# Kernel optimization log

Measured on AMD Instinct MI355X. Metric: run time of the kernel, lower is better.

Reference implementation:

```python
import jax, jax.numpy as jnp
import numpy as np

N = 4194304  # number of sequential steps (batch dim scanned over)


def setup_inputs() -> dict:
    key = jax.random.key(0)
    k1, k2, k3 = jax.random.split(key, 3)
    x = jax.random.normal(k1, (N, 1, 3), dtype=jnp.float32)
    update = jax.random.normal(k2, (N, 3, 1), dtype=jnp.float32)
    # torch init: (-1-1)*rand([3,1]) + 1  -> uniform in (-1, 1]
    network0 = -2.0 * jax.random.uniform(k3, (3, 1), dtype=jnp.float32) + 1.0
    return {"x": x, "update": update, "network0": network0}


def reference(x, update, network0):
    # state s: [3,1] fast-weight vector
    # per step: s <- sigmoid(10*(s + update_i - 0.5)); pred_i = x_i[0,:] @ s
    def step(s, inp):
        xi, ui = inp  # xi: [1,3], ui: [3,1]
        s = jax.nn.sigmoid(10.0 * (s + ui - 0.5))
        pred = (xi @ s)[0]  # [1,3]@[3,1] -> [1,1] -> [1]
        return s, pred

    _, preds = jax.lax.scan(step, network0, (x, update))
    return preds  # [N, 1]
```

## Files before the change

### kernel.cpp

```cpp
#include <hip/hip_runtime.h>

#define CH 32
#define TPB 256

__device__ __forceinline__ float sig10(float s, float u) {
    float t = (s + u) - 0.5f;
    float a = 10.0f * t;
    float e = __expf(-a);
    return 1.0f / (1.0f + e);
}

__device__ __forceinline__ void step3(float& s0, float& s1, float& s2,
                                      float u0, float u1, float u2) {
    s0 = sig10(s0, u0); s1 = sig10(s1, u1); s2 = sig10(s2, u2);
}

__global__ void __launch_bounds__(TPB, 2) p1_bracket(
    const float* __restrict__ update, float* __restrict__ state_in,
    int* __restrict__ flags, int* __restrict__ blockflags, int C, int N) {
  __shared__ int s_w[TPB / 64];
  const int tid = threadIdx.x;
  if (tid < TPB / 64) s_w[tid] = 0;
  __syncthreads();
  const int c = blockIdx.x * TPB + tid;
  const bool have = (c < C);
  const bool full = have && ((size_t)(c + 1) * CH <= (size_t)N);
  int flag = 0;
  float a0 = 0.f, a1 = 0.f, a2 = 0.f;
  if (full) {
    const float4* up4 = (const float4*)(update + (size_t)c * (CH * 3));
    float4 u[24];
#pragma unroll
    for (int g = 0; g < 24; ++g) u[g] = up4[g];
    const float lo = (c == 0) ? -1.0f : 0.0f;
    a0 = a1 = a2 = lo;
    float b0 = 1.f, b1 = 1.f, b2 = 1.f;
    bool bdone = false;
#pragma unroll
    for (int g = 0; g < 8; ++g) {
      const float4 A = u[3 * g], B = u[3 * g + 1], Cv = u[3 * g + 2];
      step3(a0, a1, a2, A.x, A.y, A.z);
      step3(a0, a1, a2, A.w, B.x, B.y);
      step3(a0, a1, a2, B.z, B.w, Cv.x);
      step3(a0, a1, a2, Cv.y, Cv.z, Cv.w);
      if (!bdone) {
        step3(b0, b1, b2, A.x, A.y, A.z);
        step3(b0, b1, b2, A.w, B.x, B.y);
        step3(b0, b1, b2, B.z, B.w, Cv.x);
        step3(b0, b1, b2, Cv.y, Cv.z, Cv.w);
        bdone = __all((a0 == b0) && (a1 == b1) && (a2 == b2));
      }
    }
    flag = bdone ? 0 : 1;
  } else if (have) {
    const float* up = update + (size_t)c * (CH * 3);
    int steps = N - c * CH;
    const float lo = (c == 0) ? -1.0f : 0.0f;
    a0 = a1 = a2 = lo;
    float b0 = 1.f, b1 = 1.f, b2 = 1.f;
    for (int i = 0; i < steps; ++i) {
      step3(a0, a1, a2, up[3 * i], up[3 * i + 1], up[3 * i + 2]);
      step3(b0, b1, b2, up[3 * i], up[3 * i + 1], up[3 * i + 2]);
    }
    flag = !((a0 == b0) && (a1 == b1) && (a2 == b2));
  }
  if (have) {
    if (c + 1 < C) {
      state_in[(size_t)(c + 1) * 3 + 0] = a0;
      state_in[(size_t)(c + 1) * 3 + 1] = a1;
      state_in[(size_t)(c + 1) * 3 + 2] = a2;
    }
    flags[c] = flag;
  }
  unsigned long long bal = __ballot(flag != 0);
  if ((tid & 63) == 0) s_w[tid >> 6] = (bal != 0ull) ? 1 : 0;
  __syncthreads();
  if (tid == 0) {
    int bf = 0;
#pragma unroll
    for (int w = 0; w < TPB / 64; ++w) bf |= s_w[w];
    blockflags[blockIdx.x] = bf;
  }
}

__global__ void p2_fix(const float* __restrict__ update,
                       const float* __restrict__ net0,
                       float* __restrict__ state_in,
                       const int* __restrict__ flags,
                       const int* __restrict__ blockflags,
                       int C, int N, int NBLK) {
  __shared__ int s_any;
  if (threadIdx.x == 0) s_any = 0;
  __syncthreads();
  int bad = 0;
  for (int i = threadIdx.x; i < NBLK; i += blockDim.x) bad |= blockflags[i];
  if (bad) atomicOr(&s_any, 1);
  __syncthreads();
  if (threadIdx.x != 0) return;
  const int any = s_any;

  float s0 = net0[0], s1 = net0[1], s2 = net0[2];
  state_in[0] = s0; state_in[1] = s1; state_in[2] = s2;
  {
    const float* up = update;
    int steps = min(CH, N);
    for (int i = 0; i < steps; ++i)
      step3(s0, s1, s2, up[3 * i], up[3 * i + 1], up[3 * i + 2]);
    if (C > 1) { state_in[3] = s0; state_in[4] = s1; state_in[5] = s2; }
  }
  if (!any) return;
  for (int blk = 0; blk < NBLK; ++blk) {
    if (!blockflags[blk]) continue;
    int cc0 = blk * TPB; if (cc0 == 0) cc0 = 1;
    int cc1 = min(blk * TPB + TPB, C);
    for (int cc = cc0; cc < cc1; ++cc) {
      if (!flags[cc]) continue;
      float t0 = state_in[(size_t)cc * 3 + 0];
      float t1 = state_in[(size_t)cc * 3 + 1];
      float t2 = state_in[(size_t)cc * 3 + 2];
      const float* up = update + (size_t)cc * (CH * 3);
      int steps = min(CH, N - cc * CH);
      for (int i = 0; i < steps; ++i)
        step3(t0, t1, t2, up[3 * i], up[3 * i + 1], up[3 * i + 2]);
      if (cc + 1 < C) {
        state_in[(size_t)(cc + 1) * 3 + 0] = t0;
        state_in[(size_t)(cc + 1) * 3 + 1] = t1;
        state_in[(size_t)(cc + 1) * 3 + 2] = t2;
      }
    }
  }
}

__global__ void __launch_bounds__(TPB, 2) p3_emit(
    const float* __restrict__ x, const float* __restrict__ update,
    const float* __restrict__ state_in, float* __restrict__ out, int C, int N) {
  __shared__ float s_out[TPB * 33];
  const int tid = threadIdx.x;
  const int c = blockIdx.x * TPB + tid;
  const bool fullBlock = ((size_t)(blockIdx.x + 1) * (TPB * CH) <= (size_t)N);
  if (fullBlock) {
    const float4* up4 = (const float4*)(update + (size_t)c * (CH * 3));
    const float4* xp4 = (const float4*)(x + (size_t)c * (CH * 3));
    float s0 = state_in[(size_t)c * 3 + 0];
    float s1 = state_in[(size_t)c * 3 + 1];
    float s2 = state_in[(size_t)c * 3 + 2];
    float4 u[24], xv[24];
#pragma unroll
    for (int g = 0; g < 24; ++g) u[g] = up4[g];
#pragma unroll
    for (int g = 0; g < 24; ++g) xv[g] = xp4[g];
#pragma unroll
    for (int g = 0; g < 8; ++g) {
      const float4 UA = u[3 * g], UB = u[3 * g + 1], UC = u[3 * g + 2];
      const float4 XA = xv[3 * g], XB = xv[3 * g + 1], XC = xv[3 * g + 2];
      float o0, o1, o2, o3;
      step3(s0, s1, s2, UA.x, UA.y, UA.z); o0 = XA.x * s0 + XA.y * s1 + XA.z * s2;
      step3(s0, s1, s2, UA.w, UB.x, UB.y); o1 = XA.w * s0 + XB.x * s1 + XB.y * s2;
      step3(s0, s1, s2, UB.z, UB.w, UC.x); o2 = XB.z * s0 + XB.w * s1 + XC.x * s2;
      step3(s0, s1, s2, UC.y, UC.z, UC.w); o3 = XC.y * s0 + XC.z * s1 + XC.w * s2;
      s_out[tid * 33 + g * 4 + 0] = o0;
      s_out[tid * 33 + g * 4 + 1] = o1;
      s_out[tid * 33 + g * 4 + 2] = o2;
      s_out[tid * 33 + g * 4 + 3] = o3;
    }
    __syncthreads();
    float* ob = out + (size_t)blockIdx.x * (TPB * CH);
#pragma unroll
    for (int k = 0; k < 32; ++k) {
      int f = k * TPB + tid;
      int t = f >> 5, idx = f & 31;
      ob[f] = s_out[t * 33 + idx];
    }
  } else if (c < C) {
    float s0 = state_in[(size_t)c * 3 + 0];
    float s1 = state_in[(size_t)c * 3 + 1];
    float s2 = state_in[(size_t)c * 3 + 2];
    const float* up = update + (size_t)c * (CH * 3);
    const float* xp = x + (size_t)c * (CH * 3);
    float* op = out + (size_t)c * CH;
    int steps = min(CH, N - c * CH);
    for (int i = 0; i < steps; ++i) {
      step3(s0, s1, s2, up[3 * i], up[3 * i + 1], up[3 * i + 2]);
      op[i] = xp[3 * i] * s0 + xp[3 * i + 1] * s1 + xp[3 * i + 2] * s2;
    }
  }
}

extern "C" void kernel_launch(void* const* d_in, const int* in_sizes, int n_in,
                              void* d_out, int out_size, void* d_ws, size_t ws_size,
                              hipStream_t stream) {
    const float* x      = (const float*)d_in[0];
    const float* update = (const float*)d_in[1];
    const float* net0   = (const float*)d_in[2];
    float* out = (float*)d_out;
    int N = out_size;
    int C = (N + CH - 1) / CH;
    int nblk = (C + TPB - 1) / TPB;

    float* state_in = (float*)d_ws;
    int* flags = (int*)((char*)d_ws + (size_t)C * 3 * sizeof(float));
    int* blockflags = flags + C;

    hipLaunchKernelGGL(p1_bracket, dim3(nblk), dim3(TPB), 0, stream,
                       update, state_in, flags, blockflags, C, N);
    hipLaunchKernelGGL(p2_fix, dim3(1), dim3(1024), 0, stream,
                       update, net0, state_in, flags, blockflags, C, N, nblk);
    hipLaunchKernelGGL(p3_emit, dim3(nblk), dim3(TPB), 0, stream,
                       x, update, state_in, out, C, N);
}
```

Baseline: 151.3 us.

## Stage update and x tiles through swizzled LDS with coalesced loads, one wave per block

Replaces the per-thread strided float4 loads (each thread reading its own 384-byte chunk) with coalesced cooperative loads of the block's whole tile into shared memory, using an XOR swizzle to avoid bank conflicts. Threads then read their chunk from LDS. Blocks shrink to a single 64-lane wave, so the block flag comes straight from the ballot and the cross-wave shared reduction goes away. This adds LDS traffic and barriers, and the p2 fix pass now scans four times as many block flags.

```diff
diff --git a/kernel.cpp b/kernel.cpp
--- a/kernel.cpp
+++ b/kernel.cpp
@@ -1,7 +1,9 @@
 #include <hip/hip_runtime.h>
 
 #define CH 32
-#define TPB 256
+#define CPB 64
+#define F4C 24
+#define TILE (CPB * F4C)
 
 __device__ __forceinline__ float sig10(float s, float u) {
     float t = (s + u) - 0.5f;
@@ -15,30 +17,38 @@
     s0 = sig10(s0, u0); s1 = sig10(s1, u1); s2 = sig10(s2, u2);
 }
 
-__global__ void __launch_bounds__(TPB, 2) p1_bracket(
+__device__ __forceinline__ int swz(int F) { return F ^ ((F / F4C) & 7); }
+
+__global__ void p1_bracket(
     const float* __restrict__ update, float* __restrict__ state_in,
     int* __restrict__ flags, int* __restrict__ blockflags, int C, int N) {
-  __shared__ int s_w[TPB / 64];
-  const int tid = threadIdx.x;
-  if (tid < TPB / 64) s_w[tid] = 0;
-  __syncthreads();
-  const int c = blockIdx.x * TPB + tid;
-  const bool have = (c < C);
-  const bool full = have && ((size_t)(c + 1) * CH <= (size_t)N);
+  __shared__ float4 su[TILE];
+  const int lane = threadIdx.x;
+  const int blk  = blockIdx.x;
+  const int c    = blk * CPB + lane;
+  const bool blockFull = ((size_t)(blk + 1) * (CPB * CH) <= (size_t)N);
   int flag = 0;
   float a0 = 0.f, a1 = 0.f, a2 = 0.f;
-  if (full) {
-    const float4* up4 = (const float4*)(update + (size_t)c * (CH * 3));
-    float4 u[24];
-#pragma unroll
-    for (int g = 0; g < 24; ++g) u[g] = up4[g];
+
+  if (blockFull) {
+    const float4* up4 = (const float4*)update + (size_t)blk * TILE;
+    float4 raw[F4C];
+#pragma unroll
+    for (int ld = 0; ld < F4C; ++ld) raw[ld] = up4[ld * CPB + lane];
+#pragma unroll
+    for (int ld = 0; ld < F4C; ++ld) su[swz(ld * CPB + lane)] = raw[ld];
+    __syncthreads();
+
     const float lo = (c == 0) ? -1.0f : 0.0f;
     a0 = a1 = a2 = lo;
     float b0 = 1.f, b1 = 1.f, b2 = 1.f;
     bool bdone = false;
+    const int base = lane * F4C;
 #pragma unroll
     for (int g = 0; g < 8; ++g) {
-      const float4 A = u[3 * g], B = u[3 * g + 1], Cv = u[3 * g + 2];
+      const float4 A  = su[swz(base + 3 * g + 0)];
+      const float4 B  = su[swz(base + 3 * g + 1)];
+      const float4 Cv = su[swz(base + 3 * g + 2)];
       step3(a0, a1, a2, A.x, A.y, A.z);
       step3(a0, a1, a2, A.w, B.x, B.y);
       step3(a0, a1, a2, B.z, B.w, Cv.x);
@@ -52,9 +62,9 @@
       }
     }
     flag = bdone ? 0 : 1;
-  } else if (have) {
+  } else if (c < C) {
     const float* up = update + (size_t)c * (CH * 3);
-    int steps = N - c * CH;
+    int steps = min(CH, N - c * CH);
     const float lo = (c == 0) ? -1.0f : 0.0f;
     a0 = a1 = a2 = lo;
     float b0 = 1.f, b1 = 1.f, b2 = 1.f;
@@ -64,7 +74,8 @@
     }
     flag = !((a0 == b0) && (a1 == b1) && (a2 == b2));
   }
-  if (have) {
+
+  if (c < C) {
     if (c + 1 < C) {
       state_in[(size_t)(c + 1) * 3 + 0] = a0;
       state_in[(size_t)(c + 1) * 3 + 1] = a1;
@@ -73,14 +84,7 @@
     flags[c] = flag;
   }
   unsigned long long bal = __ballot(flag != 0);
-  if ((tid & 63) == 0) s_w[tid >> 6] = (bal != 0ull) ? 1 : 0;
-  __syncthreads();
-  if (tid == 0) {
-    int bf = 0;
-#pragma unroll
-    for (int w = 0; w < TPB / 64; ++w) bf |= s_w[w];
-    blockflags[blockIdx.x] = bf;
-  }
+  if (lane == 0) blockflags[blk] = (bal != 0ull) ? 1 : 0;
 }
 
 __global__ void p2_fix(const float* __restrict__ update,
@@ -111,8 +115,8 @@
   if (!any) return;
   for (int blk = 0; blk < NBLK; ++blk) {
     if (!blockflags[blk]) continue;
-    int cc0 = blk * TPB; if (cc0 == 0) cc0 = 1;
-    int cc1 = min(blk * TPB + TPB, C);
+    int cc0 = blk * CPB; if (cc0 == 0) cc0 = 1;
+    int cc1 = min(blk * CPB + CPB, C);
     for (int cc = cc0; cc < cc1; ++cc) {
       if (!flags[cc]) continue;
       float t0 = state_in[(size_t)cc * 3 + 0];
@@ -131,45 +135,63 @@
   }
 }
 
-__global__ void __launch_bounds__(TPB, 2) p3_emit(
+__global__ void p3_emit(
     const float* __restrict__ x, const float* __restrict__ update,
     const float* __restrict__ state_in, float* __restrict__ out, int C, int N) {
-  __shared__ float s_out[TPB * 33];
-  const int tid = threadIdx.x;
-  const int c = blockIdx.x * TPB + tid;
-  const bool fullBlock = ((size_t)(blockIdx.x + 1) * (TPB * CH) <= (size_t)N);
-  if (fullBlock) {
-    const float4* up4 = (const float4*)(update + (size_t)c * (CH * 3));
-    const float4* xp4 = (const float4*)(x + (size_t)c * (CH * 3));
+  __shared__ float4 su[TILE];
+  __shared__ float4 sx[TILE];
+  const int lane = threadIdx.x;
+  const int blk  = blockIdx.x;
+  const int c    = blk * CPB + lane;
+  const bool blockFull = ((size_t)(blk + 1) * (CPB * CH) <= (size_t)N);
+
+  if (blockFull) {
+    const float4* up4 = (const float4*)update + (size_t)blk * TILE;
+    const float4* xp4 = (const float4*)x      + (size_t)blk * TILE;
+    float4 ru[F4C], rx[F4C];
+#pragma unroll
+    for (int ld = 0; ld < F4C; ++ld) ru[ld] = up4[ld * CPB + lane];
+#pragma unroll
+    for (int ld = 0; ld < F4C; ++ld) rx[ld] = xp4[ld * CPB + lane];
+#pragma unroll
+    for (int ld = 0; ld < F4C; ++ld) su[swz(ld * CPB + lane)] = ru[ld];
+#pragma unroll
+    for (int ld = 0; ld < F4C; ++ld) sx[swz(ld * CPB + lane)] = rx[ld];
+    __syncthreads();
+
     float s0 = state_in[(size_t)c * 3 + 0];
     float s1 = state_in[(size_t)c * 3 + 1];
     float s2 = state_in[(size_t)c * 3 + 2];
-    float4 u[24], xv[24];
-#pragma unroll
-    for (int g = 0; g < 24; ++g) u[g] = up4[g];
-#pragma unroll
-    for (int g = 0; g < 24; ++g) xv[g] = xp4[g];
+    float obuf[CH];
+    const int base = lane * F4C;
 #pragma unroll
     for (int g = 0; g < 8; ++g) {
-      const float4 UA = u[3 * g], UB = u[3 * g + 1], UC = u[3 * g + 2];
-      const float4 XA = xv[3 * g], XB = xv[3 * g + 1], XC = xv[3 * g + 2];
-      float o0, o1, o2, o3;
-      step3(s0, s1, s2, UA.x, UA.y, UA.z); o0 = XA.x * s0 + XA.y * s1 + XA.z * s2;
-      step3(s0, s1, s2, UA.w, UB.x, UB.y); o1 = XA.w * s0 + XB.x * s1 + XB.y * s2;
-      step3(s0, s1, s2, UB.z, UB.w, UC.x); o2 = XB.z * s0 + XB.w * s1 + XC.x * s2;
-      step3(s0, s1, s2, UC.y, UC.z, UC.w); o3 = XC.y * s0 + XC.z * s1 + XC.w * s2;
-      s_out[tid * 33 + g * 4 + 0] = o0;
-      s_out[tid * 33 + g * 4 + 1] = o1;
-      s_out[tid * 33 + g * 4 + 2] = o2;
-      s_out[tid * 33 + g * 4 + 3] = o3;
-    }
-    __syncthreads();
-    float* ob = out + (size_t)blockIdx.x * (TPB * CH);
-#pragma unroll
-    for (int k = 0; k < 32; ++k) {
-      int f = k * TPB + tid;
+      const float4 UA = su[swz(base + 3 * g + 0)];
+      const float4 UB = su[swz(base + 3 * g + 1)];
+      const float4 UC = su[swz(base + 3 * g + 2)];
+      const float4 XA = sx[swz(base + 3 * g + 0)];
+      const float4 XB = sx[swz(base + 3 * g + 1)];
+      const float4 XC = sx[swz(base + 3 * g + 2)];
+      step3(s0, s1, s2, UA.x, UA.y, UA.z);
+      obuf[g * 4 + 0] = XA.x * s0 + XA.y * s1 + XA.z * s2;
+      step3(s0, s1, s2, UA.w, UB.x, UB.y);
+      obuf[g * 4 + 1] = XA.w * s0 + XB.x * s1 + XB.y * s2;
+      step3(s0, s1, s2, UB.z, UB.w, UC.x);
+      obuf[g * 4 + 2] = XB.z * s0 + XB.w * s1 + XC.x * s2;
+      step3(s0, s1, s2, UC.y, UC.z, UC.w);
+      obuf[g * 4 + 3] = XC.y * s0 + XC.z * s1 + XC.w * s2;
+    }
+    __syncthreads();
+    float* s_o = (float*)su;
+#pragma unroll
+    for (int i = 0; i < CH; ++i) s_o[lane * 33 + i] = obuf[i];
+    __syncthreads();
+    float* ob = out + (size_t)blk * (CPB * CH);
+#pragma unroll
+    for (int k = 0; k < CH; ++k) {
+      int f = k * CPB + lane;
       int t = f >> 5, idx = f & 31;
-      ob[f] = s_out[t * 33 + idx];
+      ob[f] = s_o[t * 33 + idx];
     }
   } else if (c < C) {
     float s0 = state_in[(size_t)c * 3 + 0];
@@ -195,16 +217,16 @@
     float* out = (float*)d_out;
     int N = out_size;
     int C = (N + CH - 1) / CH;
-    int nblk = (C + TPB - 1) / TPB;
+    int nblk = (C + CPB - 1) / CPB;
 
     float* state_in = (float*)d_ws;
     int* flags = (int*)((char*)d_ws + (size_t)C * 3 * sizeof(float));
     int* blockflags = flags + C;
 
-    hipLaunchKernelGGL(p1_bracket, dim3(nblk), dim3(TPB), 0, stream,
+    hipLaunchKernelGGL(p1_bracket, dim3(nblk), dim3(CPB), 0, stream,
                        update, state_in, flags, blockflags, C, N);
-    hipLaunchKernelGGL(p2_fix, dim3(1), dim3(1024), 0, stream,
+    hipLaunchKernelGGL(p2_fix, dim3(1), dim3(256), 0, stream,
                        update, net0, state_in, flags, blockflags, C, N, nblk);
-    hipLaunchKernelGGL(p3_emit, dim3(nblk), dim3(TPB), 0, stream,
+    hipLaunchKernelGGL(p3_emit, dim3(nblk), dim3(CPB), 0, stream,
                        x, update, state_in, out, C, N);
 }
```

Result: slower. 168.8 us (+11.6%).

## Split emit pass into half-chunks using mid-chunk bracket states

Applied to the files above, without the earlier changes.

The bracket pass now records each chunk's state at the midpoint along with a per-lane convergence flag. The emit pass uses two threads per 32-step chunk, each handling 16 steps. When the midpoint state is known to be exact it is used directly; otherwise the thread replays the first half. This doubles thread-level parallelism in the emit pass and halves per-thread register and shared-memory use, allowing higher occupancy. The fix-up pass is simplified to a linear scan over flagged chunks, and the first chunk no longer gets a forced serial recompute. Costs are extra workspace writes and possible redundant replay when a chunk has not converged.

```diff
diff --git a/kernel.cpp b/kernel.cpp
--- a/kernel.cpp
+++ b/kernel.cpp
@@ -1,6 +1,7 @@
 #include <hip/hip_runtime.h>
 
 #define CH 32
+#define HCH 16
 #define TPB 256
 
 __device__ __forceinline__ float sig10(float s, float u) {
@@ -15,9 +16,10 @@
     s0 = sig10(s0, u0); s1 = sig10(s1, u1); s2 = sig10(s2, u2);
 }
 
-__global__ void __launch_bounds__(TPB, 2) p1_bracket(
+__global__ void __launch_bounds__(TPB, 3) p1_bracket(
     const float* __restrict__ update, float* __restrict__ state_in,
-    int* __restrict__ flags, int* __restrict__ blockflags, int C, int N) {
+    float* __restrict__ state_mid, int* __restrict__ flags,
+    int* __restrict__ midflags, int* __restrict__ blockflags, int C, int N) {
   __shared__ int s_w[TPB / 64];
   const int tid = threadIdx.x;
   if (tid < TPB / 64) s_w[tid] = 0;
@@ -25,8 +27,9 @@
   const int c = blockIdx.x * TPB + tid;
   const bool have = (c < C);
   const bool full = have && ((size_t)(c + 1) * CH <= (size_t)N);
-  int flag = 0;
+  int flag = 0, mflag = 0;
   float a0 = 0.f, a1 = 0.f, a2 = 0.f;
+  float m0 = 0.f, m1 = 0.f, m2 = 0.f;
   if (full) {
     const float4* up4 = (const float4*)(update + (size_t)c * (CH * 3));
     float4 u[24];
@@ -35,6 +38,7 @@
     const float lo = (c == 0) ? -1.0f : 0.0f;
     a0 = a1 = a2 = lo;
     float b0 = 1.f, b1 = 1.f, b2 = 1.f;
+    bool lanem = false;
     bool bdone = false;
 #pragma unroll
     for (int g = 0; g < 8; ++g) {
@@ -48,21 +52,30 @@
         step3(b0, b1, b2, A.w, B.x, B.y);
         step3(b0, b1, b2, B.z, B.w, Cv.x);
         step3(b0, b1, b2, Cv.y, Cv.z, Cv.w);
-        bdone = __all((a0 == b0) && (a1 == b1) && (a2 == b2));
-      }
-    }
-    flag = bdone ? 0 : 1;
+        bool mg = (a0 == b0) && (a1 == b1) && (a2 == b2);
+        lanem = lanem || mg;
+        bdone = __all(mg);
+      }
+      if (g == 3) {
+        m0 = a0; m1 = a1; m2 = a2;
+        mflag = lanem ? 0 : 1;
+      }
+    }
+    flag = lanem ? 0 : 1;
   } else if (have) {
     const float* up = update + (size_t)c * (CH * 3);
     int steps = N - c * CH;
     const float lo = (c == 0) ? -1.0f : 0.0f;
     a0 = a1 = a2 = lo;
     float b0 = 1.f, b1 = 1.f, b2 = 1.f;
+    bool lanem = false;
     for (int i = 0; i < steps; ++i) {
       step3(a0, a1, a2, up[3 * i], up[3 * i + 1], up[3 * i + 2]);
       step3(b0, b1, b2, up[3 * i], up[3 * i + 1], up[3 * i + 2]);
-    }
-    flag = !((a0 == b0) && (a1 == b1) && (a2 == b2));
+      lanem = lanem || ((a0 == b0) && (a1 == b1) && (a2 == b2));
+      if (i == HCH - 1) { m0 = a0; m1 = a1; m2 = a2; mflag = lanem ? 0 : 1; }
+    }
+    flag = lanem ? 0 : 1;
   }
   if (have) {
     if (c + 1 < C) {
@@ -70,7 +83,11 @@
       state_in[(size_t)(c + 1) * 3 + 1] = a1;
       state_in[(size_t)(c + 1) * 3 + 2] = a2;
     }
+    state_mid[(size_t)c * 3 + 0] = m0;
+    state_mid[(size_t)c * 3 + 1] = m1;
+    state_mid[(size_t)c * 3 + 2] = m2;
     flags[c] = flag;
+    midflags[c] = mflag;
   }
   unsigned long long bal = __ballot(flag != 0);
   if ((tid & 63) == 0) s_w[tid >> 6] = (bal != 0ull) ? 1 : 0;
@@ -97,89 +114,118 @@
   if (bad) atomicOr(&s_any, 1);
   __syncthreads();
   if (threadIdx.x != 0) return;
-  const int any = s_any;
-
-  float s0 = net0[0], s1 = net0[1], s2 = net0[2];
-  state_in[0] = s0; state_in[1] = s1; state_in[2] = s2;
-  {
-    const float* up = update;
-    int steps = min(CH, N);
+  if (!s_any) return;
+  for (int cc = 0; cc < C; ++cc) {
+    if (!flags[cc]) continue;
+    float t0, t1, t2;
+    if (cc == 0) { t0 = net0[0]; t1 = net0[1]; t2 = net0[2]; }
+    else {
+      t0 = state_in[(size_t)cc * 3 + 0];
+      t1 = state_in[(size_t)cc * 3 + 1];
+      t2 = state_in[(size_t)cc * 3 + 2];
+    }
+    const float* up = update + (size_t)cc * (CH * 3);
+    int steps = min(CH, N - cc * CH);
     for (int i = 0; i < steps; ++i)
-      step3(s0, s1, s2, up[3 * i], up[3 * i + 1], up[3 * i + 2]);
-    if (C > 1) { state_in[3] = s0; state_in[4] = s1; state_in[5] = s2; }
-  }
-  if (!any) return;
-  for (int blk = 0; blk < NBLK; ++blk) {
-    if (!blockflags[blk]) continue;
-    int cc0 = blk * TPB; if (cc0 == 0) cc0 = 1;
-    int cc1 = min(blk * TPB + TPB, C);
-    for (int cc = cc0; cc < cc1; ++cc) {
-      if (!flags[cc]) continue;
-      float t0 = state_in[(size_t)cc * 3 + 0];
-      float t1 = state_in[(size_t)cc * 3 + 1];
-      float t2 = state_in[(size_t)cc * 3 + 2];
-      const float* up = update + (size_t)cc * (CH * 3);
-      int steps = min(CH, N - cc * CH);
-      for (int i = 0; i < steps; ++i)
-        step3(t0, t1, t2, up[3 * i], up[3 * i + 1], up[3 * i + 2]);
-      if (cc + 1 < C) {
-        state_in[(size_t)(cc + 1) * 3 + 0] = t0;
-        state_in[(size_t)(cc + 1) * 3 + 1] = t1;
-        state_in[(size_t)(cc + 1) * 3 + 2] = t2;
-      }
-    }
-  }
-}
-
-__global__ void __launch_bounds__(TPB, 2) p3_emit(
+      step3(t0, t1, t2, up[3 * i], up[3 * i + 1], up[3 * i + 2]);
+    if (cc + 1 < C) {
+      state_in[(size_t)(cc + 1) * 3 + 0] = t0;
+      state_in[(size_t)(cc + 1) * 3 + 1] = t1;
+      state_in[(size_t)(cc + 1) * 3 + 2] = t2;
+    }
+  }
+}
+
+__global__ void __launch_bounds__(TPB, 3) p3_emit(
     const float* __restrict__ x, const float* __restrict__ update,
-    const float* __restrict__ state_in, float* __restrict__ out, int C, int N) {
-  __shared__ float s_out[TPB * 33];
+    const float* __restrict__ net0, const float* __restrict__ state_in,
+    const float* __restrict__ state_mid, const int* __restrict__ midflags,
+    float* __restrict__ out, int C, int N) {
+  __shared__ float s_o[TPB * 17];
   const int tid = threadIdx.x;
-  const int c = blockIdx.x * TPB + tid;
-  const bool fullBlock = ((size_t)(blockIdx.x + 1) * (TPB * CH) <= (size_t)N);
+  const int tt = blockIdx.x * TPB + tid;
+  const int c = tt >> 1, h = tt & 1;
+  const bool fullBlock = ((size_t)(blockIdx.x + 1) * (TPB * HCH) <= (size_t)N);
   if (fullBlock) {
-    const float4* up4 = (const float4*)(update + (size_t)c * (CH * 3));
-    const float4* xp4 = (const float4*)(x + (size_t)c * (CH * 3));
-    float s0 = state_in[(size_t)c * 3 + 0];
-    float s1 = state_in[(size_t)c * 3 + 1];
-    float s2 = state_in[(size_t)c * 3 + 2];
-    float4 u[24], xv[24];
-#pragma unroll
-    for (int g = 0; g < 24; ++g) u[g] = up4[g];
-#pragma unroll
-    for (int g = 0; g < 24; ++g) xv[g] = xp4[g];
-#pragma unroll
-    for (int g = 0; g < 8; ++g) {
+    const float4* up4 = (const float4*)(update + (size_t)c * (CH * 3)) + h * 12;
+    const float4* xp4 = (const float4*)(x + (size_t)c * (CH * 3)) + h * 12;
+    float4 u[12], xv[12];
+#pragma unroll
+    for (int g = 0; g < 12; ++g) u[g] = up4[g];
+#pragma unroll
+    for (int g = 0; g < 12; ++g) xv[g] = xp4[g];
+    float s0, s1, s2;
+    if (h == 0) {
+      if (c == 0) { s0 = net0[0]; s1 = net0[1]; s2 = net0[2]; }
+      else {
+        s0 = state_in[(size_t)c * 3 + 0];
+        s1 = state_in[(size_t)c * 3 + 1];
+        s2 = state_in[(size_t)c * 3 + 2];
+      }
+    } else if (midflags[c] == 0) {
+      s0 = state_mid[(size_t)c * 3 + 0];
+      s1 = state_mid[(size_t)c * 3 + 1];
+      s2 = state_mid[(size_t)c * 3 + 2];
+    } else {
+      if (c == 0) { s0 = net0[0]; s1 = net0[1]; s2 = net0[2]; }
+      else {
+        s0 = state_in[(size_t)c * 3 + 0];
+        s1 = state_in[(size_t)c * 3 + 1];
+        s2 = state_in[(size_t)c * 3 + 2];
+      }
+      const float* up = update + (size_t)c * (CH * 3);
+      for (int i = 0; i < HCH; ++i)
+        step3(s0, s1, s2, up[3 * i], up[3 * i + 1], up[3 * i + 2]);
+    }
+    float obuf[HCH];
+#pragma unroll
+    for (int g = 0; g < 4; ++g) {
       const float4 UA = u[3 * g], UB = u[3 * g + 1], UC = u[3 * g + 2];
       const float4 XA = xv[3 * g], XB = xv[3 * g + 1], XC = xv[3 * g + 2];
-      float o0, o1, o2, o3;
-      step3(s0, s1, s2, UA.x, UA.y, UA.z); o0 = XA.x * s0 + XA.y * s1 + XA.z * s2;
-      step3(s0, s1, s2, UA.w, UB.x, UB.y); o1 = XA.w * s0 + XB.x * s1 + XB.y * s2;
-      step3(s0, s1, s2, UB.z, UB.w, UC.x); o2 = XB.z * s0 + XB.w * s1 + XC.x * s2;
-      step3(s0, s1, s2, UC.y, UC.z, UC.w); o3 = XC.y * s0 + XC.z * s1 + XC.w * s2;
-      s_out[tid * 33 + g * 4 + 0] = o0;
-      s_out[tid * 33 + g * 4 + 1] = o1;
-      s_out[tid * 33 + g * 4 + 2] = o2;
-      s_out[tid * 33 + g * 4 + 3] = o3;
-    }
+      step3(s0, s1, s2, UA.x, UA.y, UA.z);
+      obuf[g * 4 + 0] = XA.x * s0 + XA.y * s1 + XA.z * s2;
+      step3(s0, s1, s2, UA.w, UB.x, UB.y);
+      obuf[g * 4 + 1] = XA.w * s0 + XB.x * s1 + XB.y * s2;
+      step3(s0, s1, s2, UB.z, UB.w, UC.x);
+      obuf[g * 4 + 2] = XB.z * s0 + XB.w * s1 + XC.x * s2;
+      step3(s0, s1, s2, UC.y, UC.z, UC.w);
+      obuf[g * 4 + 3] = XC.y * s0 + XC.z * s1 + XC.w * s2;
+    }
+#pragma unroll
+    for (int i = 0; i < HCH; ++i) s_o[tid * 17 + i] = obuf[i];
     __syncthreads();
-    float* ob = out + (size_t)blockIdx.x * (TPB * CH);
-#pragma unroll
-    for (int k = 0; k < 32; ++k) {
+    float* ob = out + (size_t)blockIdx.x * (TPB * HCH);
+#pragma unroll
+    for (int k = 0; k < HCH; ++k) {
       int f = k * TPB + tid;
-      int t = f >> 5, idx = f & 31;
-      ob[f] = s_out[t * 33 + idx];
+      ob[f] = s_o[(f >> 4) * 17 + (f & 15)];
     }
   } else if (c < C) {
-    float s0 = state_in[(size_t)c * 3 + 0];
-    float s1 = state_in[(size_t)c * 3 + 1];
-    float s2 = state_in[(size_t)c * 3 + 2];
+    int steps = min(CH, N - c * CH);
+    int i0 = h * HCH, i1 = min(steps, (h + 1) * HCH);
+    if (i0 >= i1) return;
+    float s0, s1, s2;
+    bool replay = false;
+    if (h == 0 || midflags[c] != 0) {
+      if (c == 0) { s0 = net0[0]; s1 = net0[1]; s2 = net0[2]; }
+      else {
+        s0 = state_in[(size_t)c * 3 + 0];
+        s1 = state_in[(size_t)c * 3 + 1];
+        s2 = state_in[(size_t)c * 3 + 2];
+      }
+      replay = (h == 1);
+    } else {
+      s0 = state_mid[(size_t)c * 3 + 0];
+      s1 = state_mid[(size_t)c * 3 + 1];
+      s2 = state_mid[(size_t)c * 3 + 2];
+    }
     const float* up = update + (size_t)c * (CH * 3);
     const float* xp = x + (size_t)c * (CH * 3);
     float* op = out + (size_t)c * CH;
-    int steps = min(CH, N - c * CH);
-    for (int i = 0; i < steps; ++i) {
+    if (replay)
+      for (int i = 0; i < i0; ++i)
+        step3(s0, s1, s2, up[3 * i], up[3 * i + 1], up[3 * i + 2]);
+    for (int i = i0; i < i1; ++i) {
       step3(s0, s1, s2, up[3 * i], up[3 * i + 1], up[3 * i + 2]);
       op[i] = xp[3 * i] * s0 + xp[3 * i + 1] * s1 + xp[3 * i + 2] * s2;
     }
@@ -195,16 +241,22 @@
     float* out = (float*)d_out;
     int N = out_size;
     int C = (N + CH - 1) / CH;
-    int nblk = (C + TPB - 1) / TPB;
-
-    float* state_in = (float*)d_ws;
-    int* flags = (int*)((char*)d_ws + (size_t)C * 3 * sizeof(float));
-    int* blockflags = flags + C;
-
-    hipLaunchKernelGGL(p1_bracket, dim3(nblk), dim3(TPB), 0, stream,
-                       update, state_in, flags, blockflags, C, N);
-    hipLaunchKernelGGL(p2_fix, dim3(1), dim3(1024), 0, stream,
-                       update, net0, state_in, flags, blockflags, C, N, nblk);
-    hipLaunchKernelGGL(p3_emit, dim3(nblk), dim3(TPB), 0, stream,
-                       x, update, state_in, out, C, N);
-}
+    int nblk1 = (C + TPB - 1) / TPB;
+    int nblk3 = (2 * C + TPB - 1) / TPB;
+
+    char* w = (char*)d_ws;
+    float* state_in  = (float*)w;                         w += (size_t)C * 3 * 4;
+    float* state_mid = (float*)w;                         w += (size_t)C * 3 * 4;
+    int* flags       = (int*)w;                           w += (size_t)C * 4;
+    int* midflags    = (int*)w;                           w += (size_t)C * 4;
+    int* blockflags  = (int*)w;
+
+    hipLaunchKernelGGL(p1_bracket, dim3(nblk1), dim3(TPB), 0, stream,
+                       update, state_in, state_mid, flags, midflags,
+                       blockflags, C, N);
+    hipLaunchKernelGGL(p2_fix, dim3(1), dim3(TPB), 0, stream,
+                       update, net0, state_in, flags, blockflags, C, N, nblk1);
+    hipLaunchKernelGGL(p3_emit, dim3(nblk3), dim3(TPB), 0, stream,
+                       x, update, net0, state_in, state_mid, midflags,
+                       out, C, N);
+}
```

Result: faster. 145.1 us (-4.1%).
